# Kernel optimization log

Measured on AMD Instinct MI355X. Metric: run time of the kernel, lower is better.

## Reference

```python
import jax, jax.numpy as jnp
import numpy as np

B, QL, D = 4, 1024, 1024
H, HD = 16, 64
KVL = 2048


def setup_inputs() -> dict:
    key = jax.random.key(0)
    ks = jax.random.split(key, 6)
    scale = 1.0 / np.sqrt(D)
    return {
        "hidden_states": jax.random.normal(ks[0], (B, QL, D), dtype=jnp.float32),
        "key_states": jax.random.normal(ks[1], (B, H, KVL, HD), dtype=jnp.float32),
        "value_states": jax.random.normal(ks[2], (B, H, KVL, HD), dtype=jnp.float32),
        "attention_mask": jnp.zeros((B, 1, 1, KVL), dtype=jnp.float32),
        "Wq": jax.random.normal(ks[3], (D, D), dtype=jnp.float32) * scale,
        "Wo": jax.random.normal(ks[4], (D, D), dtype=jnp.float32) * scale,
    }


def reference(hidden_states, key_states, value_states, attention_mask, Wq, Wo):
    batch = hidden_states.shape[0]
    # Q projection (T5 Linear has no bias), split heads: [B, H, Q, HD]
    q = jnp.einsum("bqd,de->bqe", hidden_states, Wq)
    q = q.reshape(batch, -1, H, HD).transpose(0, 2, 1, 3)
    # NOTE: T5 attention has NO 1/sqrt(d) scaling
    scores = jnp.einsum("bhqd,bhkd->bhqk", q, key_states) + attention_mask
    attn = jax.nn.softmax(scores.astype(jnp.float32), axis=-1).astype(scores.dtype)
    out = jnp.einsum("bhqk,bhkd->bhqd", attn, value_states)
    out = out.transpose(0, 2, 1, 3).reshape(batch, -1, H * HD)
    return jnp.einsum("bqe,ed->bqd", out, Wo)
```

## Files before the change

kernel.cpp:

```cpp
#include <hip/hip_runtime.h>
#include <hip/hip_bf16.h>
#include <hip/hip_fp16.h>
#include <stdint.h>

typedef _Float16 f16;
typedef _Float16 f16x2 __attribute__((ext_vector_type(2)));
typedef _Float16 f16x4 __attribute__((ext_vector_type(4)));
typedef _Float16 f16x8 __attribute__((ext_vector_type(8)));
typedef float f32x4 __attribute__((ext_vector_type(4)));
typedef float f32x16 __attribute__((ext_vector_type(16)));
typedef uint32_t u32x4 __attribute__((ext_vector_type(4)));

#define B_ 4
#define QL_ 1024
#define D_ 1024
#define H_ 16
#define HD_ 64
#define KVL_ 2048
#define L2E 1.44269504088896f

__device__ __forceinline__ void g2lds16(const void* g, void* l) {
    __builtin_amdgcn_global_load_lds(
        (const __attribute__((address_space(1))) uint32_t*)g,
        (__attribute__((address_space(3))) uint32_t*)l,
        16, 0, 0);
}

union U8 { uint32_t u[4]; f16x8 v; };

__device__ __forceinline__ uint32_t pkrtz(float a, float b) {
    auto t = __builtin_amdgcn_cvt_pkrtz(a, b);
    return __builtin_bit_cast(uint32_t, t);
}

__global__ void prep_wq(const float* __restrict__ Wq, f16* __restrict__ Wq_t) {
    __shared__ float t[64][65];
    int b2 = blockIdx.x, tid = threadIdx.x;
    int k0 = (b2 >> 4) << 6, n0 = (b2 & 15) << 6;
    int rr = tid >> 4, c4 = (tid & 15) << 2;
#pragma unroll
    for (int i = 0; i < 4; ++i) {
        int r = i * 16 + rr;
        float4 v = *(const float4*)(Wq + (size_t)(k0 + r) * 1024 + n0 + c4);
        t[r][c4 + 0] = v.x; t[r][c4 + 1] = v.y; t[r][c4 + 2] = v.z; t[r][c4 + 3] = v.w;
    }
    __syncthreads();
#pragma unroll
    for (int i = 0; i < 4; ++i) {
        int n = i * 16 + rr;
        f16x4 o;
#pragma unroll
        for (int j = 0; j < 4; ++j) o[j] = (f16)t[c4 + j][n];
        *(f16x4*)(Wq_t + (size_t)(n0 + n) * 1024 + k0 + c4) = o;
    }
}

__global__ __launch_bounds__(512) void gemm0_fused(
    const float* __restrict__ hs, const f16* __restrict__ BT, f16* __restrict__ q_h,
    const float* __restrict__ K, f16* __restrict__ K_h,
    const float* __restrict__ V, f16* __restrict__ V_t,
    const float* __restrict__ Wo, f16* __restrict__ Wo_t,
    const float* __restrict__ mask, f16* __restrict__ em16) {
    __shared__ char shmem[49152];
    int bid = blockIdx.x, tid = threadIdx.x;

    if (bid < 512) {
        char* Alds = shmem;
        char* Blds = shmem + 32768;
        int xcd = bid & 7, sx = bid >> 3;
        int bm = xcd * 4 + (sx & 3);
        int bn = sx >> 2;
        int w = tid >> 6, l = tid & 63;
        int l15 = l & 15, lg = l >> 4;
        int wm = w >> 1, wn = w & 1;
        f32x4 acc[2][2] = {};

        int rA0 = tid >> 3, c80 = tid & 7, cc0 = c80 ^ (rA0 & 7);
        const float* ags0 = hs + ((size_t)(bm * 128 + rA0) * 1024 + cc0 * 8);
        const float* ags1 = ags0 + 65536;
        int aw0 = rA0 * 128 + c80 * 16;
        int aw1 = aw0 + 8192;

        int rB = w * 8 + (l >> 3);
        int ccB = (l & 7) ^ (rB & 7);
        const char* bgp = (const char*)BT + ((size_t)(bn * 64 + rB) * 1024 + ccB * 8) * 2;
        int boB = w * 1024;

        int aoff[2][2], boff[2][2];
#pragma unroll
        for (int ks = 0; ks < 2; ++ks)
#pragma unroll
            for (int m = 0; m < 2; ++m) {
                int ra = wm * 32 + m * 16 + l15;
                aoff[ks][m] = ra * 128 + ((ks * 64 + lg * 16) ^ ((ra & 7) << 4));
                int rb = wn * 32 + m * 16 + l15;
                boff[ks][m] = rb * 128 + ((ks * 64 + lg * 16) ^ ((rb & 7) << 4));
            }

        f32x4 a0, a1, a2, a3;
#define ALOAD(buf, o32, oB)                                    \
    {                                                          \
        a0 = *(const f32x4*)(ags0 + (o32));                    \
        a1 = *(const f32x4*)(ags0 + (o32) + 4);                \
        a2 = *(const f32x4*)(ags1 + (o32));                    \
        a3 = *(const f32x4*)(ags1 + (o32) + 4);                \
        g2lds16(bgp + (oB), Blds + (buf) * 8192 + boB);        \
    }
#define CVTW(buf)                                                              \
    {                                                                          \
        asm volatile("s_waitcnt vmcnt(1)" ::: "memory");                       \
        u32x4 w0 = { pkrtz(a0[0], a0[1]), pkrtz(a0[2], a0[3]),                 \
                     pkrtz(a1[0], a1[1]), pkrtz(a1[2], a1[3]) };               \
        *(u32x4*)(Alds + (buf) * 16384 + aw0) = w0;                            \
        u32x4 w1 = { pkrtz(a2[0], a2[1]), pkrtz(a2[2], a2[3]),                 \
                     pkrtz(a3[0], a3[1]), pkrtz(a3[2], a3[3]) };               \
        *(u32x4*)(Alds + (buf) * 16384 + aw1) = w1;                            \
    }
#define GCOMP(buf)                                                               \
    _Pragma("unroll") for (int ks = 0; ks < 2; ++ks) {                           \
        f16x8 af[2], bf[2];                                                      \
        af[0] = *(const f16x8*)(Alds + (buf) * 16384 + aoff[ks][0]);             \
        af[1] = *(const f16x8*)(Alds + (buf) * 16384 + aoff[ks][1]);             \
        bf[0] = *(const f16x8*)(Blds + (buf) * 8192 + boff[ks][0]);              \
        bf[1] = *(const f16x8*)(Blds + (buf) * 8192 + boff[ks][1]);              \
        _Pragma("unroll") for (int m = 0; m < 2; ++m)                            \
            _Pragma("unroll") for (int n = 0; n < 2; ++n)                        \
                acc[m][n] = __builtin_amdgcn_mfma_f32_16x16x32_f16(af[m], bf[n], acc[m][n], 0, 0, 0); \
    }
#define SYNCV()                                                          \
    {                                                                    \
        asm volatile("s_waitcnt vmcnt(0) lgkmcnt(0)" ::: "memory");      \
        __syncthreads();                                                 \
    }

        ALOAD(0, 0, 0);
        CVTW(0);
        SYNCV();
        for (int t2 = 0; t2 < 8; ++t2) {
            ALOAD(1, 64, 128);
            GCOMP(0);
            CVTW(1);
            SYNCV();
            if (t2 < 7) ALOAD(0, 128, 256);
            GCOMP(1);
            if (t2 < 7) CVTW(0);
            SYNCV();
            ags0 += 128; ags1 += 128; bgp += 256;
        }
#pragma unroll
        for (int m = 0; m < 2; ++m)
#pragma unroll
            for (int n = 0; n < 2; ++n)
#pragma unroll
                for (int i = 0; i < 4; ++i) {
                    int row = bm * 128 + wm * 32 + m * 16 + lg * 4 + i;
                    int col = bn * 64 + wn * 32 + n * 16 + l15;
                    float v = acc[m][n][i] * L2E;
                    int b = row >> 10, q = row & 1023, h = col >> 6, d = col & 63;
                    q_h[(((size_t)b * H_ + h) * QL_ + q) * HD_ + d] = (f16)v;
                }
#undef ALOAD
#undef CVTW
#undef GCOMP
#undef SYNCV
    } else if (bid < 1536) {
        int t0 = (bid - 512) * 512 + tid;
#pragma unroll
        for (int rep = 0; rep < 2; ++rep) {
            int U = t0 + rep * 524288;
            int bh = U >> 14, rem = U & 16383;
            int ch = rem >> 9, r2 = rem & 511;
            int dsl = r2 >> 7, r3 = r2 & 127;
            int kv = r3 >> 1, hi2 = r3 & 1;
            const float* sp = K + (((size_t)bh * KVL_ + ch * 64 + kv) * HD_ + dsl * 16 + hi2 * 8);
            f16x8 o;
#pragma unroll
            for (int j = 0; j < 8; ++j) o[j] = (f16)sp[j];
            *(f16x8*)(K_h + (size_t)U * 8) = o;
        }
    } else if (bid < 2560) {
        int sub = tid >> 8, st2 = tid & 255;
        int vb = (bid - 1536) * 2 + sub;
        int bh = vb >> 5, ch = vb & 31;
        int b = bh >> 4;
        float (*tt)[65] = (float(*)[65])(shmem + sub * 16640);
        float* emv = (float*)(shmem + 33280 + sub * 256);
        int rr = st2 >> 4, c4 = (st2 & 15) << 2;
#pragma unroll
        for (int i = 0; i < 4; ++i) {
            int r = i * 16 + rr;
            float4 v = *(const float4*)(V + ((size_t)bh * KVL_ + ch * 64 + r) * HD_ + c4);
            tt[r][c4 + 0] = v.x; tt[r][c4 + 1] = v.y; tt[r][c4 + 2] = v.z; tt[r][c4 + 3] = v.w;
        }
        if (st2 < 64)
            emv[st2] = __builtin_amdgcn_exp2f(mask[(size_t)b * KVL_ + ch * 64 + st2] * L2E);
        __syncthreads();
#pragma unroll
        for (int rep = 0; rep < 2; ++rep) {
            int u = st2 + rep * 256;
            int st = u >> 7, d = (u >> 1) & 63, hi2 = u & 1;
            f16x8 o;
#pragma unroll
            for (int j = 0; j < 8; ++j) {
                int kvl = st * 16 + (j & 3) + 8 * (j >> 2) + 4 * hi2;
                o[j] = (f16)(tt[kvl][d] * emv[kvl]);
            }
            *(f16x8*)(V_t + ((size_t)(bh * 32 + ch) * 512 + u) * 8) = o;
        }
        if (((bh & 15) == 0) && st2 < 64) {
            int kb = st2 >> 5, hi2v = (st2 >> 4) & 1, slot = st2 & 15;
            int kvv = kb * 32 + (slot & 3) + 8 * (slot >> 2) + 4 * hi2v;
            em16[(((size_t)b * 64 + ch * 2 + kb) * 2 + hi2v) * 16 + slot] = (f16)emv[kvv];
        }
    } else {
        int sub = tid >> 8, st2 = tid & 255;
        int b2 = (bid - 2560) * 2 + sub;
        float (*tt)[65] = (float(*)[65])(shmem + sub * 16640);
        int k0 = (b2 >> 4) << 6, n0 = (b2 & 15) << 6;
        int rr = st2 >> 4, c4 = (st2 & 15) << 2;
#pragma unroll
        for (int i = 0; i < 4; ++i) {
            int r = i * 16 + rr;
            float4 v = *(const float4*)(Wo + (size_t)(k0 + r) * 1024 + n0 + c4);
            tt[r][c4 + 0] = v.x; tt[r][c4 + 1] = v.y; tt[r][c4 + 2] = v.z; tt[r][c4 + 3] = v.w;
        }
        __syncthreads();
#pragma unroll
        for (int i = 0; i < 4; ++i) {
            int n = i * 16 + rr;
            f16x4 o;
#pragma unroll
            for (int j = 0; j < 4; ++j) o[j] = (f16)tt[c4 + j][n];
            *(f16x4*)(Wo_t + (size_t)(n0 + n) * 1024 + k0 + c4) = o;
        }
    }
}

__global__ __launch_bounds__(512) void gemm_tn1(
    const f16* __restrict__ A, const f16* __restrict__ BT, float* __restrict__ Cout) {
    __shared__ char Alds[2][16384];
    __shared__ char Blds[2][8192];
    int d0 = blockIdx.x;
    int xcd = d0 & 7, sx = d0 >> 3;
    int bm = xcd * 4 + (sx & 3);
    int bn = sx >> 2;
    int tid = threadIdx.x, w = tid >> 6, l = tid & 63;
    int l15 = l & 15, lg = l >> 4;
    int wm = w >> 1, wn = w & 1;
    f32x4 acc[2][2] = {};

    const char* ag0; const char* ag1; int ao0, ao1;
    {
        int i0 = w, i1 = w + 8;
        int r0 = i0 * 8 + (l >> 3), r1 = i1 * 8 + (l >> 3);
        int c0 = (l & 7) ^ (r0 & 7), c1 = (l & 7) ^ (r1 & 7);
        ag0 = (const char*)A + ((size_t)(bm * 128 + r0) * 1024 + c0 * 8) * 2;
        ag1 = (const char*)A + ((size_t)(bm * 128 + r1) * 1024 + c1 * 8) * 2;
        ao0 = i0 * 1024; ao1 = i1 * 1024;
    }
    int rB = w * 8 + (l >> 3);
    int ccB = (l & 7) ^ (rB & 7);
    const char* bgp = (const char*)BT + ((size_t)(bn * 64 + rB) * 1024 + ccB * 8) * 2;
    int boB = w * 1024;

    int aoff[2][2], boff[2][2];
#pragma unroll
    for (int ks = 0; ks < 2; ++ks)
#pragma unroll
        for (int m = 0; m < 2; ++m) {
            int ra = wm * 32 + m * 16 + l15;
            aoff[ks][m] = ra * 128 + ((ks * 64 + lg * 16) ^ ((ra & 7) << 4));
            int rb = wn * 32 + m * 16 + l15;
            boff[ks][m] = rb * 128 + ((ks * 64 + lg * 16) ^ ((rb & 7) << 4));
        }
    const char* Ab = &Alds[0][0];
    const char* Bb = &Blds[0][0];

#define GSTAGE(buf, soff)                                      \
    {                                                          \
        g2lds16(ag0 + (soff), &Alds[buf][ao0]);                \
        g2lds16(ag1 + (soff), &Alds[buf][ao1]);                \
        g2lds16(bgp + (soff), &Blds[buf][boB]);                \
    }
#define GCOMP(buf)                                                               \
    _Pragma("unroll") for (int ks = 0; ks < 2; ++ks) {                           \
        f16x8 af[2], bf[2];                                                      \
        af[0] = *(const f16x8*)(Ab + (buf) * 16384 + aoff[ks][0]);               \
        af[1] = *(const f16x8*)(Ab + (buf) * 16384 + aoff[ks][1]);               \
        bf[0] = *(const f16x8*)(Bb + (buf) * 8192 + boff[ks][0]);                \
        bf[1] = *(const f16x8*)(Bb + (buf) * 8192 + boff[ks][1]);                \
        _Pragma("unroll") for (int m = 0; m < 2; ++m)                            \
            _Pragma("unroll") for (int n = 0; n < 2; ++n)                        \
                acc[m][n] = __builtin_amdgcn_mfma_f32_16x16x32_f16(af[m], bf[n], acc[m][n], 0, 0, 0); \
    }

    GSTAGE(0, 0);
    asm volatile("s_waitcnt vmcnt(0)" ::: "memory");
    __syncthreads();
    for (int t2 = 0; t2 < 8; ++t2) {
        GSTAGE(1, 128);
        GCOMP(0);
        asm volatile("s_waitcnt vmcnt(0)" ::: "memory");
        __syncthreads();
        if (t2 < 7) GSTAGE(0, 256);
        GCOMP(1);
        asm volatile("s_waitcnt vmcnt(0)" ::: "memory");
        __syncthreads();
        ag0 += 256; ag1 += 256; bgp += 256;
    }
#pragma unroll
    for (int m = 0; m < 2; ++m)
#pragma unroll
        for (int n = 0; n < 2; ++n)
#pragma unroll
            for (int i = 0; i < 4; ++i) {
                int row = bm * 128 + wm * 32 + m * 16 + lg * 4 + i;
                int col = bn * 64 + wn * 32 + n * 16 + l15;
                Cout[(size_t)row * 1024 + col] = acc[m][n][i];
            }
#undef GSTAGE
#undef GCOMP
}

__global__ __launch_bounds__(256, 2) void attn_fused(
    const f16* __restrict__ qh, const f16* __restrict__ kh, const f16* __restrict__ vt,
    const f16* __restrict__ em16, f16* __restrict__ aout) {
    __shared__ char exch[16384];
    __shared__ char em_lds[4096];
    __shared__ float frl[4][32];
    __shared__ float fr2[2][2][32];
    __shared__ float2 msx[2][32];

    int tid = threadIdx.x, w = tid >> 6, l = tid & 63;
    int l31 = l & 31, hi = l >> 5;
    int g = w >> 1, qsub = w & 1;
    int d0 = blockIdx.x;
    int xcd = d0 & 7, sx = d0 >> 3;
    int bh = xcd * 8 + (sx & 7);
    int qt = sx >> 3;
    int b = bh >> 4, h = bh & 15;

    const char* embase = em_lds + hi * 32;

    f16x8 Qf[4];
    {
        const f16* qp = qh + ((size_t)bh * QL_ + qt * 64 + qsub * 32 + l31) * HD_ + hi * 8;
#pragma unroll
        for (int ds_ = 0; ds_ < 4; ++ds_) Qf[ds_] = *(const f16x8*)(qp + ds_ * 16);
    }

    const char* kgp = (const char*)kh + (size_t)(bh * 32 + g * 16) * 8192 + l31 * 32 + hi * 16;
    const char* vgp = (const char*)vt + (size_t)(bh * 32 + g * 16) * 8192 + l31 * 32 + hi * 16;

#define LOADK(dst, off)                                              \
    {                                                                \
        _Pragma("unroll") for (int i_ = 0; i_ < 4; ++i_)             \
            dst[i_] = *(const f16x8*)(kgp + (off) + i_ * 2048);      \
    }
#define LOADV(dst, off)                                              \
    {                                                                \
        _Pragma("unroll") for (int i_ = 0; i_ < 4; ++i_)             \
            dst[i_] = *(const f16x8*)(vgp + (off) + i_ * 1024);      \
    }

    float mrun = -1e30f, ssA = 0.f, ssB = 0.f;
    f32x16 acc[2] = {};
    int emoff = g * 2048;

#define BODY(Kf, Vf, emo)                                                                 \
    {                                                                                     \
        f32x16 St = {};                                                                   \
        __builtin_amdgcn_s_setprio(1);                                                    \
        _Pragma("unroll") for (int ds_ = 0; ds_ < 4; ++ds_)                               \
            St = __builtin_amdgcn_mfma_f32_32x32x16_f16(Kf[ds_], Qf[ds_], St, 0, 0, 0);   \
        __builtin_amdgcn_s_setprio(0);                                                    \
        float a0 = fmaxf(fmaxf(St[0], St[1]), St[2]);                                     \
        float a1 = fmaxf(fmaxf(St[3], St[4]), St[5]);                                     \
        float a2 = fmaxf(fmaxf(St[6], St[7]), St[8]);                                     \
        float a3 = fmaxf(fmaxf(St[9], St[10]), St[11]);                                   \
        float a4 = fmaxf(fmaxf(St[12], St[13]), St[14]);                                  \
        float lmax = fmaxf(fmaxf(fmaxf(a0, a1), St[15]), fmaxf(a2, fmaxf(a3, a4)));       \
        if (__any(lmax > mrun + 12.f)) {                                                  \
            float pm = fmaxf(lmax, __shfl_xor(lmax, 32));                                 \
            float mn = fmaxf(mrun, pm);                                                   \
            float fac = __builtin_amdgcn_exp2f(mrun - mn);                                \
            mrun = mn; ssA *= fac; ssB *= fac;                                            \
            frl[w][l31] = fac;                                                            \
            asm volatile("s_waitcnt lgkmcnt(0)" ::: "memory");                            \
            _Pragma("unroll") for (int g4 = 0; g4 < 4; ++g4) {                            \
                f32x4 fv = *(const f32x4*)&frl[w][g4 * 8 + hi * 4];                       \
                _Pragma("unroll") for (int c = 0; c < 2; ++c)                             \
                    _Pragma("unroll") for (int j = 0; j < 4; ++j)                         \
                        acc[c][g4 * 4 + j] *= fv[j];                                      \
            }                                                                             \
        }                                                                                 \
        uint32_t pk[8];                                                                   \
        _Pragma("unroll") for (int i = 0; i < 8; ++i) {                                   \
            float p0 = __builtin_amdgcn_exp2f(St[2 * i] - mrun);                          \
            float p1 = __builtin_amdgcn_exp2f(St[2 * i + 1] - mrun);                      \
            pk[i] = pkrtz(p0, p1);                                                        \
        }                                                                                 \
        __builtin_amdgcn_s_setprio(1);                                                    \
        _Pragma("unroll") for (int sti = 0; sti < 2; ++sti) {                             \
            U8 pa;                                                                        \
            pa.u[0] = pk[sti * 4 + 0]; pa.u[1] = pk[sti * 4 + 1];                         \
            pa.u[2] = pk[sti * 4 + 2]; pa.u[3] = pk[sti * 4 + 3];                         \
            _Pragma("unroll") for (int c = 0; c < 2; ++c)                                 \
                acc[c] = __builtin_amdgcn_mfma_f32_32x32x16_f16(pa.v, Vf[sti * 2 + c], acc[c], 0, 0, 0); \
        }                                                                                 \
        __builtin_amdgcn_s_setprio(0);                                                    \
        U8 ea, eb;                                                                        \
        ea.v = *(const f16x8*)(embase + (emo));                                           \
        eb.v = *(const f16x8*)(embase + (emo) + 16);                                      \
        _Pragma("unroll") for (int i = 0; i < 4; ++i) {                                   \
            ssA = __builtin_amdgcn_fdot2(__builtin_bit_cast(f16x2, pk[2 * i]),            \
                                         __builtin_bit_cast(f16x2, (2 * i) < 4 ? ea.u[2 * i] : eb.u[2 * i - 4]), ssA, false); \
            ssB = __builtin_amdgcn_fdot2(__builtin_bit_cast(f16x2, pk[2 * i + 1]),        \
                                         __builtin_bit_cast(f16x2, (2 * i + 1) < 4 ? ea.u[2 * i + 1] : eb.u[2 * i - 3]), ssB, false); \
        }                                                                                 \
    }

    g2lds16((const char*)em16 + b * 4096 + w * 1024 + l * 16, em_lds + w * 1024);
    f16x8 Ka[4], Kb[4], Va[4], Vb[4];
    LOADK(Ka, 0);
    asm volatile("s_waitcnt vmcnt(0)" ::: "memory");
    __syncthreads();

    for (int it = 0; it < 16; ++it) {
        LOADV(Va, 0);
        LOADK(Kb, 1024);
        BODY(Ka, Va, emoff);
        LOADV(Vb, 4096);
        if (it < 15) LOADK(Ka, 8192);
        BODY(Kb, Vb, emoff + 64);
        kgp += 8192; vgp += 8192; emoff += 128;
    }

    float ssum = ssA + ssB;
    ssum += __shfl_xor(ssum, 32);
    __syncthreads();
    if (g == 1) {
        int base = qsub * 8192 + l * 128;
#pragma unroll
        for (int i = 0; i < 8; ++i) {
            int c = i >> 2, j0 = (i & 3) * 4;
            f32x4 vv = { acc[c][j0], acc[c][j0 + 1], acc[c][j0 + 2], acc[c][j0 + 3] };
            *(f32x4*)(exch + base + ((i * 16) ^ ((l & 7) << 4))) = vv;
        }
        if (hi == 0) msx[qsub][l31] = make_float2(mrun, ssum);
    }
    __syncthreads();
    if (g == 0) {
        float2 mb = msx[qsub][l31];
        float m = fmaxf(mrun, mb.x);
        float fA = __builtin_amdgcn_exp2f(mrun - m);
        float fB = __builtin_amdgcn_exp2f(mb.x - m);
        float s = ssum * fA + mb.y * fB;
        float rinv = 1.0f / s;
        if (hi == 0) { fr2[qsub][0][l31] = fA * rinv; fr2[qsub][1][l31] = fB * rinv; }
        asm volatile("s_waitcnt lgkmcnt(0)" ::: "memory");
        int base = qsub * 8192 + l * 128;
#pragma unroll
        for (int c = 0; c < 2; ++c)
#pragma unroll
            for (int g4 = 0; g4 < 4; ++g4) {
                f32x4 gAv = *(const f32x4*)&fr2[qsub][0][g4 * 8 + hi * 4];
                f32x4 gBv = *(const f32x4*)&fr2[qsub][1][g4 * 8 + hi * 4];
                int i = c * 4 + g4;
                f32x4 pv = *(const f32x4*)(exch + base + ((i * 16) ^ ((l & 7) << 4)));
#pragma unroll
                for (int j = 0; j < 4; ++j) {
                    float o = acc[c][g4 * 4 + j] * gAv[j] + pv[j] * gBv[j];
                    int q = qt * 64 + qsub * 32 + g4 * 8 + hi * 4 + j;
                    int dd = c * 32 + l31;
                    aout[((size_t)b * QL_ + q) * D_ + h * HD_ + dd] = (f16)o;
                }
            }
    }
#undef LOADK
#undef LOADV
#undef BODY
}

extern "C" void kernel_launch(void* const* d_in, const int* in_sizes, int n_in,
                              void* d_out, int out_size, void* d_ws, size_t ws_size,
                              hipStream_t stream) {
    const float* hs = (const float*)d_in[0];
    const float* K  = (const float*)d_in[1];
    const float* V  = (const float*)d_in[2];
    const float* mask = (const float*)d_in[3];
    const float* Wq = (const float*)d_in[4];
    const float* Wo = (const float*)d_in[5];
    float* out = (float*)d_out;
    char* ws = (char*)d_ws;

    f16* Wq_t = (f16*)(ws + 0);
    f16* Wo_t = (f16*)(ws + 2097152);
    f16* K_h  = (f16*)(ws + 4194304);
    f16* V_t  = (f16*)(ws + 20971520);
    f16* q_h  = (f16*)(ws + 37748736);
    f16* a_o  = (f16*)(ws + 46137344);
    f16* em16 = (f16*)(ws + 54525952);

    prep_wq<<<256, 256, 0, stream>>>(Wq, Wq_t);
    gemm0_fused<<<2688, 512, 0, stream>>>(hs, Wq_t, q_h, K, K_h, V, V_t,
                                          Wo, Wo_t, mask, em16);
    attn_fused<<<1024, 256, 0, stream>>>(q_h, K_h, V_t, em16, a_o);
    gemm_tn1<<<512, 512, 0, stream>>>(a_o, Wo_t, out);
}
```

Baseline: 109.0 us.

## Hand-schedule K/V global loads with inline asm and explicit vmcnt waits

Replaces the compiler-generated K/V fragment loads in the attention main loop with inline-asm global_load_dwordx4 instructions that use immediate offsets. Explicit partial s_waitcnt vmcnt counts, paired with sched barriers, let each block of MFMAs wait only on the loads it needs, so the next K and V tiles stay in flight during the current softmax and PV work. A single V buffer replaces the two, and the last iteration is peeled. The compiler cannot see that these asm loads are asynchronous, so correctness depends entirely on the hand-written wait counts and barriers, and the fixed scheduling may limit the compiler's own interleaving.

```diff
diff --git a/kernel.cpp b/kernel.cpp
--- a/kernel.cpp
+++ b/kernel.cpp
@@ -349,20 +349,19 @@
         for (int ds_ = 0; ds_ < 4; ++ds_) Qf[ds_] = *(const f16x8*)(qp + ds_ * 16);
     }
 
-    const char* kgp = (const char*)kh + (size_t)(bh * 32 + g * 16) * 8192 + l31 * 32 + hi * 16;
-    const char* vgp = (const char*)vt + (size_t)(bh * 32 + g * 16) * 8192 + l31 * 32 + hi * 16;
-
-#define LOADK(dst, off)                                              \
-    {                                                                \
-        _Pragma("unroll") for (int i_ = 0; i_ < 4; ++i_)             \
-            dst[i_] = *(const f16x8*)(kgp + (off) + i_ * 2048);      \
-    }
-#define LOADV(dst, off)                                              \
-    {                                                                \
-        _Pragma("unroll") for (int i_ = 0; i_ < 4; ++i_)             \
-            dst[i_] = *(const f16x8*)(vgp + (off) + i_ * 1024);      \
-    }
-
+    const char* kA = (const char*)kh + (size_t)(bh * 32 + g * 16) * 8192 + l31 * 32 + hi * 16;
+    const char* kB = kA + 4096;
+    const char* vA = (const char*)vt + (size_t)(bh * 32 + g * 16) * 8192 + l31 * 32 + hi * 16;
+    const char* vB = vA + 4096;
+
+#define GLOAD(dst, base, offlit)                                               \
+    asm volatile("global_load_dwordx4 %0, %1, off offset:" offlit              \
+                 : "=v"(dst) : "v"(base))
+#define WAITV(nlit)                                                            \
+    { asm volatile("s_waitcnt vmcnt(" nlit ")" ::: "memory");                  \
+      __builtin_amdgcn_sched_barrier(0); }
+
+    u32x4 ka[4], kb[4], va[4];
     float mrun = -1e30f, ssA = 0.f, ssB = 0.f;
     f32x16 acc[2] = {};
     int emoff = g * 2048;
@@ -372,7 +371,8 @@
         f32x16 St = {};                                                                   \
         __builtin_amdgcn_s_setprio(1);                                                    \
         _Pragma("unroll") for (int ds_ = 0; ds_ < 4; ++ds_)                               \
-            St = __builtin_amdgcn_mfma_f32_32x32x16_f16(Kf[ds_], Qf[ds_], St, 0, 0, 0);   \
+            St = __builtin_amdgcn_mfma_f32_32x32x16_f16(                                  \
+                __builtin_bit_cast(f16x8, Kf[ds_]), Qf[ds_], St, 0, 0, 0);                \
         __builtin_amdgcn_s_setprio(0);                                                    \
         float a0 = fmaxf(fmaxf(St[0], St[1]), St[2]);                                     \
         float a1 = fmaxf(fmaxf(St[3], St[4]), St[5]);                                     \
@@ -400,13 +400,15 @@
             float p1 = __builtin_amdgcn_exp2f(St[2 * i + 1] - mrun);                      \
             pk[i] = pkrtz(p0, p1);                                                        \
         }                                                                                 \
+        WAITV("4");                                                                       \
         __builtin_amdgcn_s_setprio(1);                                                    \
         _Pragma("unroll") for (int sti = 0; sti < 2; ++sti) {                             \
             U8 pa;                                                                        \
             pa.u[0] = pk[sti * 4 + 0]; pa.u[1] = pk[sti * 4 + 1];                         \
             pa.u[2] = pk[sti * 4 + 2]; pa.u[3] = pk[sti * 4 + 3];                         \
             _Pragma("unroll") for (int c = 0; c < 2; ++c)                                 \
-                acc[c] = __builtin_amdgcn_mfma_f32_32x32x16_f16(pa.v, Vf[sti * 2 + c], acc[c], 0, 0, 0); \
+                acc[c] = __builtin_amdgcn_mfma_f32_32x32x16_f16(                          \
+                    pa.v, __builtin_bit_cast(f16x8, Vf[sti * 2 + c]), acc[c], 0, 0, 0);   \
         }                                                                                 \
         __builtin_amdgcn_s_setprio(0);                                                    \
         U8 ea, eb;                                                                        \
@@ -421,19 +423,43 @@
     }
 
     g2lds16((const char*)em16 + b * 4096 + w * 1024 + l * 16, em_lds + w * 1024);
-    f16x8 Ka[4], Kb[4], Va[4], Vb[4];
-    LOADK(Ka, 0);
     asm volatile("s_waitcnt vmcnt(0)" ::: "memory");
     __syncthreads();
 
-    for (int it = 0; it < 16; ++it) {
-        LOADV(Va, 0);
-        LOADK(Kb, 1024);
-        BODY(Ka, Va, emoff);
-        LOADV(Vb, 4096);
-        if (it < 15) LOADK(Ka, 8192);
-        BODY(Kb, Vb, emoff + 64);
-        kgp += 8192; vgp += 8192; emoff += 128;
+    GLOAD(ka[0], kA, "0");    GLOAD(ka[1], kA, "2048");
+    GLOAD(ka[2], kB, "0");    GLOAD(ka[3], kB, "2048");
+
+    for (int it = 0; it < 15; ++it) {
+        GLOAD(va[0], vA, "0");    GLOAD(va[1], vA, "1024");
+        GLOAD(va[2], vA, "2048"); GLOAD(va[3], vA, "3072");
+        GLOAD(kb[0], kA, "1024"); GLOAD(kb[1], kA, "3072");
+        GLOAD(kb[2], kB, "1024"); GLOAD(kb[3], kB, "3072");
+        WAITV("8");
+        BODY(ka, va, emoff);
+        GLOAD(va[0], vB, "0");    GLOAD(va[1], vB, "1024");
+        GLOAD(va[2], vB, "2048"); GLOAD(va[3], vB, "3072");
+        kA += 8192; kB += 8192; vA += 8192; vB += 8192;
+        GLOAD(ka[0], kA, "0");    GLOAD(ka[1], kA, "2048");
+        GLOAD(ka[2], kB, "0");    GLOAD(ka[3], kB, "2048");
+        WAITV("8");
+        BODY(kb, va, emoff + 64);
+        emoff += 128;
+    }
+    {
+        GLOAD(va[0], vA, "0");    GLOAD(va[1], vA, "1024");
+        GLOAD(va[2], vA, "2048"); GLOAD(va[3], vA, "3072");
+        GLOAD(kb[0], kA, "1024"); GLOAD(kb[1], kA, "3072");
+        GLOAD(kb[2], kB, "1024"); GLOAD(kb[3], kB, "3072");
+        WAITV("8");
+        BODY(ka, va, emoff);
+        GLOAD(va[0], vB, "0");    GLOAD(va[1], vB, "1024");
+        GLOAD(va[2], vB, "2048"); GLOAD(va[3], vB, "3072");
+        WAITV("4");
+        {
+            asm volatile("s_waitcnt vmcnt(0)" ::: "memory");
+            __builtin_amdgcn_sched_barrier(0);
+            BODY(kb, va, emoff + 64);
+        }
     }
 
     float ssum = ssA + ssB;
@@ -477,8 +503,8 @@
                 }
             }
     }
-#undef LOADK
-#undef LOADV
+#undef GLOAD
+#undef WAITV
 #undef BODY
 }
 
```

New measurement: 108.4 us. About the same (-0.6%).
